# Kernel optimization log

Hardware: AMD Instinct MI355X
Metric: run time of the kernel (lower is better)

Reference implementation:

```python
import jax, jax.numpy as jnp
import numpy as np

N, D, K = 32768, 256, 8192
SQRT3 = 3.0 ** 0.5


def setup_inputs() -> dict:
    key = jax.random.key(0)
    k1, k2 = jax.random.split(key)
    x = jax.random.normal(k1, (N, D), dtype=jnp.float32)
    # torch .uniform_(-sqrt(3), sqrt(3)) on an [D, K] table
    embeddings = jax.random.uniform(k2, (D, K), dtype=jnp.float32,
                                    minval=-SQRT3, maxval=SQRT3)
    return {"x": x, "embeddings": embeddings}


def reference(x, embeddings):
    # x: [N, D] (forward flattens from dim 1; 2D input is identity)
    # embeddings: [D, K]
    # squared L2 distances: ||y||^2 - 2 y.E + ||e||^2  -> [N, K]
    dist = (jnp.sum(x * x, axis=1, keepdims=True)
            - 2.0 * (x @ embeddings)
            + jnp.sum(embeddings * embeddings, axis=0, keepdims=True))
    idx = jnp.argmin(dist, axis=1)  # [N]
    # one_hot(idx) @ E^T == gather of columns of E (same math, no dense one-hot)
    quantized = jnp.take(embeddings, idx, axis=1).T  # [N, D]
    return quantized.reshape(x.shape)
```

## Files before the change

### kernel.cpp

```cpp
#include <hip/hip_runtime.h>
#include <math.h>
#include <float.h>

#define N_ROWS 32768
#define D_DIM  256
#define K_DIM  8192

#define EPS1 0.40f
#define EPS2 0.02f
#define T2CAP 4096
#define T3CAP 512
#define NSPLIT3 16

typedef _Float16 f16;
typedef _Float16 f16x8 __attribute__((ext_vector_type(8)));
typedef float f32x4 __attribute__((ext_vector_type(4)));

#define KSPLIT 8
#define COLS_PER_SPLIT (K_DIM / KSPLIT)
#define CHUNK_COLS 32
#define NCHUNK (COLS_PER_SPLIT / CHUNK_COLS)

__global__ void convx_kernel(const float* __restrict__ X, f16* __restrict__ X16) {
    const size_t i = ((size_t)blockIdx.x * 256 + threadIdx.x) * 8;
    float4 a = *reinterpret_cast<const float4*>(X + i);
    float4 b = *reinterpret_cast<const float4*>(X + i + 4);
    f16x8 o;
    o[0]=(f16)a.x; o[1]=(f16)a.y; o[2]=(f16)a.z; o[3]=(f16)a.w;
    o[4]=(f16)b.x; o[5]=(f16)b.y; o[6]=(f16)b.z; o[7]=(f16)b.w;
    *reinterpret_cast<f16x8*>(X16 + i) = o;
}

__global__ void packe_kernel(const float* __restrict__ E, f16* __restrict__ Epack) {
    const int gid = blockIdx.x * 256 + threadIdx.x;
    const int l    = gid & 63;
    const int t    = (gid >> 6) & 7;
    const int tile = gid >> 9;
    const int k  = 16 * tile + (l & 15);
    const int d0 = 32 * t + (l >> 4) * 8;
    f16x8 o;
#pragma unroll
    for (int j = 0; j < 8; ++j) o[j] = (f16)E[(size_t)(d0 + j) * K_DIM + k];
    *reinterpret_cast<f16x8*>(Epack + (size_t)gid * 8) = o;
}

__global__ void nhen_kernel(const float* __restrict__ E, float* __restrict__ nhen) {
    const int k = blockIdx.x * 256 + threadIdx.x;
    float s = 0.0f;
#pragma unroll 8
    for (int d = 0; d < D_DIM; ++d) {
        float v = E[(size_t)d * K_DIM + k];
        s = fmaf(v, v, s);
    }
    nhen[k] = -0.5f * s;
}

__global__ void transpose_kernel(const float* __restrict__ E, float* __restrict__ ET) {
    __shared__ float t[64][65];
    const int bk = blockIdx.x & (K_DIM / 64 - 1);
    const int bd = blockIdx.x >> 7;
    const int c  = threadIdx.x & 63;
    const int r0 = (threadIdx.x >> 6) * 16;
    const int d0 = bd * 64, k0 = bk * 64;
#pragma unroll
    for (int i = 0; i < 16; ++i)
        t[r0 + i][c] = E[(size_t)(d0 + r0 + i) * K_DIM + k0 + c];
    __syncthreads();
#pragma unroll
    for (int i = 0; i < 16; ++i)
        ET[(size_t)(k0 + r0 + i) * D_DIM + d0 + c] = t[c][r0 + i];
}

__launch_bounds__(256, 2)
__global__ void pass1_kernel(const f16* __restrict__ X16,
                             const f16* __restrict__ Epack,
                             const float* __restrict__ nhen,
                             float* __restrict__ p_best,
                             float* __restrict__ p_sec,
                             int*   __restrict__ p_idx) {
    __shared__ f16 B_lds[2][8192];

    const int tid = threadIdx.x;
    const int wv = tid >> 6;
    const int lane = tid & 63;
    const int l15 = lane & 15;
    const int l4  = lane >> 4;
    const int rg = blockIdx.x >> 3;
    const int ks = blockIdx.x & 7;
    const int rowW = rg * 256 + wv * 64;
    const int colBase = ks * COLS_PER_SPLIT;

    f16x8 A[4][8];
#pragma unroll
    for (int rt = 0; rt < 4; ++rt)
#pragma unroll
        for (int t = 0; t < 8; ++t)
            A[rt][t] = *reinterpret_cast<const f16x8*>(
                X16 + (size_t)(rowW + 16*rt + l15) * D_DIM + 32*t + l4*8);

    float best[16], sec[16];
    int bbase[16];
#pragma unroll
    for (int s = 0; s < 16; ++s) { best[s] = -INFINITY; sec[s] = -INFINITY; bbase[s] = 0; }

    const float4* src = reinterpret_cast<const float4*>(
        Epack + (size_t)colBase * 256);

    float4 sreg[4];
#pragma unroll
    for (int q = 0; q < 4; ++q) sreg[q] = src[q*256 + tid];
    {
        float4* bw = reinterpret_cast<float4*>(&B_lds[0][0]);
#pragma unroll
        for (int q = 0; q < 4; ++q) bw[q*256 + tid] = sreg[q];
    }

    for (int ci = 0; ci < NCHUNK; ++ci) {
        __syncthreads();
        if (ci + 1 < NCHUNK) {
#pragma unroll
            for (int q = 0; q < 4; ++q)
                sreg[q] = src[(size_t)(ci+1)*1024 + q*256 + tid];
        }
        const f16* bufc = &B_lds[ci & 1][0];
        const int c0 = colBase + ci * CHUNK_COLS;

#pragma unroll
        for (int ct = 0; ct < 2; ++ct) {
            const float nh = nhen[c0 + 16*ct + l15];
            const f32x4 nh4 = {nh, nh, nh, nh};
            f32x4 acc[4];
            {
                f16x8 B = *reinterpret_cast<const f16x8*>(bufc + (ct*8)*512 + lane*8);
#pragma unroll
                for (int rt = 0; rt < 4; ++rt)
                    acc[rt] = __builtin_amdgcn_mfma_f32_16x16x32_f16(A[rt][0], B, nh4, 0, 0, 0);
            }
#pragma unroll
            for (int t = 1; t < 8; ++t) {
                f16x8 B = *reinterpret_cast<const f16x8*>(bufc + (ct*8 + t)*512 + lane*8);
#pragma unroll
                for (int rt = 0; rt < 4; ++rt)
                    acc[rt] = __builtin_amdgcn_mfma_f32_16x16x32_f16(A[rt][t], B, acc[rt], 0, 0, 0);
            }
#pragma unroll
            for (int rt = 0; rt < 4; ++rt) {
#pragma unroll
                for (int r = 0; r < 4; ++r) {
                    const float v = acc[rt][r];
                    const int sl = rt*4 + r;
                    sec[sl] = __builtin_amdgcn_fmed3f(v, best[sl], sec[sl]);
                    const bool gt = v > best[sl];
                    best[sl] = gt ? v : best[sl];
                    bbase[sl] = gt ? (c0 + 16*ct) : bbase[sl];
                }
            }
        }

        if (ci + 1 < NCHUNK) {
            float4* bw = reinterpret_cast<float4*>(&B_lds[(ci+1) & 1][0]);
#pragma unroll
            for (int q = 0; q < 4; ++q) bw[q*256 + tid] = sreg[q];
        }
    }

#pragma unroll
    for (int s = 0; s < 16; ++s) {
        float b = best[s], sc = sec[s];
        int k = bbase[s] + l15;
#pragma unroll
        for (int off = 8; off >= 1; off >>= 1) {
            float ob = __shfl_xor(b, off, 16);
            float os = __shfl_xor(sc, off, 16);
            int   ok = __shfl_xor(k, off, 16);
            float sm = fmaxf(fmaxf(sc, os), fminf(b, ob));
            bool take = (ob > b) || (ob == b && ok < k);
            b = take ? ob : b;
            k = take ? ok : k;
            sc = sm;
        }
        if (l15 == 0) {
            const int row = rowW + 16*(s >> 2) + 4*l4 + (s & 3);
            p_best[ks * N_ROWS + row] = b;
            p_sec [ks * N_ROWS + row] = sc;
            p_idx [ks * N_ROWS + row] = k;
        }
    }
}

__global__ void zero_counts_kernel(int* count, int* count3) { *count = 0; *count3 = 0; }

__global__ void merge_kernel(const float* __restrict__ p_best,
                             const float* __restrict__ p_sec,
                             const int*   __restrict__ p_idx,
                             int* __restrict__ idxf,
                             int* __restrict__ list, int* __restrict__ count) {
    const int n = blockIdx.x * 256 + threadIdx.x;
    float b = p_best[n], sc = p_sec[n];
    int k = p_idx[n];
#pragma unroll
    for (int s = 1; s < KSPLIT; ++s) {
        float ob = p_best[s * N_ROWS + n];
        float os = p_sec [s * N_ROWS + n];
        int   ok = p_idx [s * N_ROWS + n];
        float sm = fmaxf(fmaxf(sc, os), fminf(b, ob));
        bool take = ob > b;
        b = take ? ob : b; k = take ? ok : k; sc = sm;
    }
    idxf[n] = k;
    if (2.0f * (b - sc) < EPS1) {
        int pos = atomicAdd(count, 1);
        if (pos < T2CAP) list[pos] = n;
    }
}

__launch_bounds__(256, 2)
__global__ void tier2_kernel(const float* __restrict__ X,
                             const float* __restrict__ E,
                             const float* __restrict__ nhen,
                             const int* __restrict__ list,
                             const int* __restrict__ count,
                             float* __restrict__ t2b, float* __restrict__ t2s,
                             int* __restrict__ t2i) {
    const int g  = blockIdx.x >> 4;
    const int sp = blockIdx.x & 15;
    const int cnt = min(*count, T2CAP);
    if (g * 64 >= cnt) return;

    __shared__ float xT[D_DIM][64];
    __shared__ float es[64][64];
    const int tid = threadIdx.x;
    const int tx = tid & 15, ty = tid >> 4;

    {
        const int r = tid >> 2;
        const int slot = min(g * 64 + r, cnt - 1);
        const int row = list[slot];
        const int d0 = (tid & 3) * 64;
        const float* xp = X + (size_t)row * D_DIM + d0;
#pragma unroll
        for (int i = 0; i < 64; i += 4) {
            float4 v = *reinterpret_cast<const float4*>(xp + i);
            xT[d0+i+0][r] = v.x; xT[d0+i+1][r] = v.y;
            xT[d0+i+2][r] = v.z; xT[d0+i+3][r] = v.w;
        }
    }

    float best[4], sec[4]; int bidx[4];
#pragma unroll
    for (int i = 0; i < 4; ++i) { best[i] = -INFINITY; sec[i] = -INFINITY; bidx[i] = 0; }

    const int colBase = sp * 512;
    for (int kc = 0; kc < 512; kc += 64) {
        float acc[4][4];
#pragma unroll
        for (int i = 0; i < 4; ++i)
#pragma unroll
            for (int j = 0; j < 4; ++j) acc[i][j] = 0.0f;

        for (int dc = 0; dc < D_DIM; dc += 64) {
            __syncthreads();
#pragma unroll
            for (int dd = 0; dd < 64; dd += 16) {
                int d = dd + (tid >> 4);
                float4 v = *reinterpret_cast<const float4*>(
                    &E[(size_t)(dc + d) * K_DIM + colBase + kc + (tid & 15) * 4]);
                *reinterpret_cast<float4*>(&es[d][(tid & 15) * 4]) = v;
            }
            __syncthreads();
#pragma unroll 8
            for (int d = 0; d < 64; ++d) {
                float4 xv = *reinterpret_cast<const float4*>(&xT[dc + d][ty * 4]);
                float4 ev = *reinterpret_cast<const float4*>(&es[d][tx * 4]);
                float xr[4] = {xv.x, xv.y, xv.z, xv.w};
                float ec[4] = {ev.x, ev.y, ev.z, ev.w};
#pragma unroll
                for (int i = 0; i < 4; ++i)
#pragma unroll
                    for (int j = 0; j < 4; ++j)
                        acc[i][j] = fmaf(xr[i], ec[j], acc[i][j]);
            }
        }
        float4 nhv = *reinterpret_cast<const float4*>(&nhen[colBase + kc + tx * 4]);
        float nh[4] = {nhv.x, nhv.y, nhv.z, nhv.w};
#pragma unroll
        for (int j = 0; j < 4; ++j) {
            const int k = colBase + kc + tx * 4 + j;
#pragma unroll
            for (int i = 0; i < 4; ++i) {
                float u = nh[j] + acc[i][j];
                bool gt = u > best[i];
                sec[i]  = fmaxf(sec[i], fminf(u, best[i]));
                best[i] = gt ? u : best[i];
                bidx[i] = gt ? k : bidx[i];
            }
        }
    }

#pragma unroll
    for (int off = 8; off >= 1; off >>= 1) {
#pragma unroll
        for (int i = 0; i < 4; ++i) {
            float ob = __shfl_xor(best[i], off, 16);
            float os = __shfl_xor(sec[i], off, 16);
            int   ok = __shfl_xor(bidx[i], off, 16);
            float sm = fmaxf(fmaxf(sec[i], os), fminf(best[i], ob));
            bool take = (ob > best[i]) || (ob == best[i] && ok < bidx[i]);
            best[i] = take ? ob : best[i];
            bidx[i] = take ? ok : bidx[i];
            sec[i] = sm;
        }
    }
    if (tx == 0) {
#pragma unroll
        for (int i = 0; i < 4; ++i) {
            const int slot = g * 64 + ty * 4 + i;
            if (slot < cnt) {
                t2b[sp * T2CAP + slot] = best[i];
                t2s[sp * T2CAP + slot] = sec[i];
                t2i[sp * T2CAP + slot] = bidx[i];
            }
        }
    }
}

__global__ void merge2_kernel(const float* __restrict__ t2b,
                              const float* __restrict__ t2s,
                              const int*   __restrict__ t2i,
                              const int* __restrict__ list,
                              const int* __restrict__ count,
                              int* __restrict__ idxf,
                              int* __restrict__ list3, int* __restrict__ count3) {
    const int slot = blockIdx.x * 256 + threadIdx.x;
    const int cnt = min(*count, T2CAP);
    if (slot >= cnt) return;
    float b = t2b[slot], sc = t2s[slot];
    int k = t2i[slot];
#pragma unroll
    for (int sp = 1; sp < 16; ++sp) {
        float ob = t2b[sp * T2CAP + slot];
        float os = t2s[sp * T2CAP + slot];
        int   ok = t2i[sp * T2CAP + slot];
        float sm = fmaxf(fmaxf(sc, os), fminf(b, ob));
        bool take = ob > b;
        b = take ? ob : b; k = take ? ok : k; sc = sm;
    }
    const int n = list[slot];
    idxf[n] = k;
    if (2.0f * (b - sc) < EPS2) {
        int pos = atomicAdd(count3, 1);
        if (pos < T3CAP) list3[pos] = n;
    }
}

__launch_bounds__(256)
__global__ void tier3_kernel(const float* __restrict__ X,
                             const float* __restrict__ E,
                             const int* __restrict__ list3,
                             const int* __restrict__ count3,
                             double* __restrict__ t3b, int* __restrict__ t3i) {
    const int slot = blockIdx.x >> 4;
    const int sp   = blockIdx.x & 15;
    const int cnt = min(*count3, T3CAP);
    if (slot >= cnt) return;
    const int n = list3[slot];

    __shared__ float xs[D_DIM];
    const int tid = threadIdx.x;
    xs[tid] = X[(size_t)n * D_DIM + tid];
    __syncthreads();

    const int colBase = sp * 512;
    double best = DBL_MAX;
    int bi = 0x7fffffff;
#pragma unroll
    for (int kk = 0; kk < 512; kk += 256) {
        const int k = colBase + kk + tid;
        double s0 = 0.0, s1 = 0.0, s2 = 0.0, s3 = 0.0;
#pragma unroll 4
        for (int d = 0; d < D_DIM; d += 4) {
            double f0 = (double)xs[d+0] - (double)E[(size_t)(d+0) * K_DIM + k];
            double f1 = (double)xs[d+1] - (double)E[(size_t)(d+1) * K_DIM + k];
            double f2 = (double)xs[d+2] - (double)E[(size_t)(d+2) * K_DIM + k];
            double f3 = (double)xs[d+3] - (double)E[(size_t)(d+3) * K_DIM + k];
            s0 = fma(f0, f0, s0); s1 = fma(f1, f1, s1);
            s2 = fma(f2, f2, s2); s3 = fma(f3, f3, s3);
        }
        double s = (s0 + s1) + (s2 + s3);
        if (s < best) { best = s; bi = k; }
    }

    __shared__ double bv[256];
    __shared__ int bix[256];
    bv[tid] = best; bix[tid] = bi;
    __syncthreads();
    if (tid == 0) {
        double b = bv[0]; int ix = bix[0];
        for (int t = 1; t < 256; ++t)
            if (bv[t] < b || (bv[t] == b && bix[t] < ix)) { b = bv[t]; ix = bix[t]; }
        t3b[sp * T3CAP + slot] = b;
        t3i[sp * T3CAP + slot] = ix;
    }
}

__global__ void merge3_kernel(const double* __restrict__ t3b,
                              const int* __restrict__ t3i,
                              const int* __restrict__ list3,
                              const int* __restrict__ count3,
                              int* __restrict__ idxf) {
    const int slot = blockIdx.x * 256 + threadIdx.x;
    const int cnt = min(*count3, T3CAP);
    if (slot >= cnt) return;
    double b = t3b[slot];
    int k = t3i[slot];
#pragma unroll
    for (int sp = 1; sp < NSPLIT3; ++sp) {
        double ob = t3b[sp * T3CAP + slot];
        int   ok = t3i[sp * T3CAP + slot];
        if (ob < b || (ob == b && ok < k)) { b = ob; k = ok; }
    }
    idxf[list3[slot]] = k;
}

__global__ void gather2_kernel(const float* __restrict__ ET,
                               const int* __restrict__ idx,
                               float* __restrict__ out) {
    const int n  = blockIdx.x * 4 + (threadIdx.x >> 6);
    const int d4 = (threadIdx.x & 63) * 4;
    const int k  = idx[n];
    *reinterpret_cast<float4*>(&out[(size_t)n * D_DIM + d4]) =
        *reinterpret_cast<const float4*>(&ET[(size_t)k * D_DIM + d4]);
}

__global__ void gather_kernel(const float* __restrict__ E,
                              const int* __restrict__ idx,
                              float* __restrict__ out) {
    const int n = blockIdx.x;
    const int d = threadIdx.x;
    const int k = idx[n];
    out[(size_t)n * D_DIM + d] = E[(size_t)d * K_DIM + k];
}

__global__ void fb_enorm_kernel(const float* __restrict__ E, float* __restrict__ enorm) {
    int k = blockIdx.x * 256 + threadIdx.x;
    float s = 0.0f;
#pragma unroll 8
    for (int d = 0; d < D_DIM; ++d) { float v = E[(size_t)d * K_DIM + k]; s = fmaf(v, v, s); }
    enorm[k] = s;
}

__launch_bounds__(256, 2)
__global__ void fb_dist_kernel(const float* __restrict__ X, const float* __restrict__ E,
                               const float* __restrict__ enorm,
                               int* __restrict__ idx_out, float* __restrict__ gap_out) {
    __shared__ float xT[D_DIM][64];
    __shared__ float es[64][64];
    const int tid = threadIdx.x;
    const int tx = tid & 15, ty = tid >> 4;
    const int rowBase = blockIdx.x * 64;
    {
        const int r = tid >> 2;
        const int d0 = (tid & 3) * 64;
        const float* xp = X + (size_t)(rowBase + r) * D_DIM + d0;
#pragma unroll
        for (int i = 0; i < 64; i += 4) {
            float4 v = *reinterpret_cast<const float4*>(xp + i);
            xT[d0+i+0][r]=v.x; xT[d0+i+1][r]=v.y; xT[d0+i+2][r]=v.z; xT[d0+i+3][r]=v.w;
        }
    }
    float bestVal[4], secVal[4]; int bestIdx[4];
#pragma unroll
    for (int i = 0; i < 4; ++i) { bestVal[i]=INFINITY; secVal[i]=INFINITY; bestIdx[i]=0; }
    for (int kc = 0; kc < K_DIM; kc += 64) {
        float acc[4][4];
#pragma unroll
        for (int i=0;i<4;++i)
#pragma unroll
            for (int j=0;j<4;++j) acc[i][j]=0.f;
        for (int dc = 0; dc < D_DIM; dc += 64) {
            __syncthreads();
#pragma unroll
            for (int dd = 0; dd < 64; dd += 16) {
                int d = dd + (tid >> 4);
                float4 v = *reinterpret_cast<const float4*>(
                    &E[(size_t)(dc+d)*K_DIM + kc + (tid&15)*4]);
                *reinterpret_cast<float4*>(&es[d][(tid&15)*4]) = v;
            }
            __syncthreads();
#pragma unroll 8
            for (int d = 0; d < 64; ++d) {
                float4 xv = *reinterpret_cast<const float4*>(&xT[dc+d][ty*4]);
                float4 ev = *reinterpret_cast<const float4*>(&es[d][tx*4]);
                float xr[4]={xv.x,xv.y,xv.z,xv.w}, ec[4]={ev.x,ev.y,ev.z,ev.w};
#pragma unroll
                for (int i=0;i<4;++i)
#pragma unroll
                    for (int j=0;j<4;++j) acc[i][j]=fmaf(xr[i],ec[j],acc[i][j]);
            }
        }
        float4 env = *reinterpret_cast<const float4*>(&enorm[kc + tx*4]);
        float en[4]={env.x,env.y,env.z,env.w};
#pragma unroll
        for (int j=0;j<4;++j) {
            int k = kc + tx*4 + j;
#pragma unroll
            for (int i=0;i<4;++i) {
                float s = fmaf(-2.0f, acc[i][j], en[j]);
                if (s < bestVal[i]) { secVal[i]=bestVal[i]; bestVal[i]=s; bestIdx[i]=k; }
                else if (s < secVal[i]) secVal[i]=s;
            }
        }
    }
#pragma unroll
    for (int off=8; off>=1; off>>=1) {
#pragma unroll
        for (int i=0;i<4;++i) {
            float oB=__shfl_xor(bestVal[i],off,16);
            int oI=__shfl_xor(bestIdx[i],off,16);
            float oS=__shfl_xor(secVal[i],off,16);
            float ms=fminf(fminf(secVal[i],oS),fmaxf(bestVal[i],oB));
            if (oB<bestVal[i] || (oB==bestVal[i] && oI<bestIdx[i])) { bestVal[i]=oB; bestIdx[i]=oI; }
            secVal[i]=ms;
        }
    }
    if (tx==0) {
#pragma unroll
        for (int i=0;i<4;++i) {
            idx_out[rowBase + ty*4 + i] = bestIdx[i];
            gap_out[rowBase + ty*4 + i] = secVal[i]-bestVal[i];
        }
    }
}

__launch_bounds__(256)
__global__ void fb_refine_kernel(const float* __restrict__ X, const float* __restrict__ E,
                                 const float* __restrict__ gap, int* __restrict__ idx) {
    const int n = blockIdx.x;
    if (gap[n] >= 0.0625f) return;
    __shared__ float xs[D_DIM];
    const int tid = threadIdx.x;
    xs[tid] = X[(size_t)n * D_DIM + tid];
    __syncthreads();
    double best = DBL_MAX; int bi = 0x7fffffff;
    for (int k = tid; k < K_DIM; k += 256) {
        double s0=0,s1=0,s2=0,s3=0;
#pragma unroll 4
        for (int d = 0; d < D_DIM; d += 4) {
            double f0=(double)xs[d+0]-(double)E[(size_t)(d+0)*K_DIM+k];
            double f1=(double)xs[d+1]-(double)E[(size_t)(d+1)*K_DIM+k];
            double f2=(double)xs[d+2]-(double)E[(size_t)(d+2)*K_DIM+k];
            double f3=(double)xs[d+3]-(double)E[(size_t)(d+3)*K_DIM+k];
            s0=fma(f0,f0,s0); s1=fma(f1,f1,s1); s2=fma(f2,f2,s2); s3=fma(f3,f3,s3);
        }
        double s=(s0+s1)+(s2+s3);
        if (s<best){best=s;bi=k;}
    }
    __shared__ double bv[256]; __shared__ int bix[256];
    bv[tid]=best; bix[tid]=bi;
    __syncthreads();
    if (tid==0) {
        double b=bv[0]; int ix=bix[0];
        for (int t=1;t<256;++t)
            if (bv[t]<b || (bv[t]==b && bix[t]<ix)) { b=bv[t]; ix=bix[t]; }
        idx[n]=ix;
    }
}

extern "C" void kernel_launch(void* const* d_in, const int* in_sizes, int n_in,
                              void* d_out, int out_size, void* d_ws, size_t ws_size,
                              hipStream_t stream) {
    const float* X = (const float*)d_in[0];
    const float* E = (const float*)d_in[1];
    float* out = (float*)d_out;
    char* ws = (char*)d_ws;

    const size_t o_nhen  = 0;
    const size_t o_pb    = 32768;
    const size_t o_ps    = o_pb  + (size_t)KSPLIT * N_ROWS * 4;
    const size_t o_pi    = o_ps  + (size_t)KSPLIT * N_ROWS * 4;
    const size_t o_idx   = o_pi  + (size_t)KSPLIT * N_ROWS * 4;
    const size_t o_list  = o_idx + (size_t)N_ROWS * 4;
    const size_t o_count = o_list + (size_t)T2CAP * 4;
    const size_t o_t2b   = o_count + 256;
    const size_t o_t2s   = o_t2b + (size_t)16 * T2CAP * 4;
    const size_t o_t2i   = o_t2s + (size_t)16 * T2CAP * 4;
    const size_t o_list3 = o_t2i + (size_t)16 * T2CAP * 4;
    const size_t o_t3b   = o_list3 + (size_t)T3CAP * 4;
    const size_t o_t3i   = o_t3b + (size_t)NSPLIT3 * T3CAP * 8;
    const size_t o_x16   = o_t3i + (size_t)NSPLIT3 * T3CAP * 4;
    const size_t o_epack = o_x16 + (size_t)N_ROWS * D_DIM * 2;
    const size_t NEED_BASE = o_epack + (size_t)D_DIM * K_DIM * 2;
    const size_t o_et    = NEED_BASE;
    const size_t NEED_FULL = o_et + (size_t)D_DIM * K_DIM * 4;

    if (ws_size >= NEED_BASE) {
        float*  nhen  = (float*) (ws + o_nhen);
        float*  p_b   = (float*) (ws + o_pb);
        float*  p_s   = (float*) (ws + o_ps);
        int*    p_i   = (int*)   (ws + o_pi);
        int*    idxf  = (int*)   (ws + o_idx);
        int*    list  = (int*)   (ws + o_list);
        int*    count = (int*)   (ws + o_count);
        int*    count3= (int*)   (ws + o_count + 4);
        float*  t2b   = (float*) (ws + o_t2b);
        float*  t2s   = (float*) (ws + o_t2s);
        int*    t2i   = (int*)   (ws + o_t2i);
        int*    list3 = (int*)   (ws + o_list3);
        double* t3b   = (double*)(ws + o_t3b);
        int*    t3i   = (int*)   (ws + o_t3i);
        f16*    X16   = (f16*)   (ws + o_x16);
        f16*    Epack = (f16*)   (ws + o_epack);
        float*  ET    = (float*) (ws + o_et);
        const bool haveET = ws_size >= NEED_FULL;

        convx_kernel<<<(N_ROWS * D_DIM / 8) / 256, 256, 0, stream>>>(X, X16);
        packe_kernel<<<(K_DIM / 16) * 8 * 64 / 256, 256, 0, stream>>>(E, Epack);
        nhen_kernel<<<K_DIM / 256, 256, 0, stream>>>(E, nhen);
        if (haveET)
            transpose_kernel<<<(K_DIM / 64) * (D_DIM / 64), 256, 0, stream>>>(E, ET);
        zero_counts_kernel<<<1, 1, 0, stream>>>(count, count3);
        pass1_kernel<<<(N_ROWS / 256) * KSPLIT, 256, 0, stream>>>(
            X16, Epack, nhen, p_b, p_s, p_i);
        merge_kernel<<<N_ROWS / 256, 256, 0, stream>>>(
            p_b, p_s, p_i, idxf, list, count);
        tier2_kernel<<<(T2CAP / 64) * 16, 256, 0, stream>>>(
            X, E, nhen, list, count, t2b, t2s, t2i);
        merge2_kernel<<<T2CAP / 256, 256, 0, stream>>>(
            t2b, t2s, t2i, list, count, idxf, list3, count3);
        tier3_kernel<<<T3CAP * NSPLIT3, 256, 0, stream>>>(
            X, E, list3, count3, t3b, t3i);
        merge3_kernel<<<T3CAP / 256, 256, 0, stream>>>(
            t3b, t3i, list3, count3, idxf);
        if (haveET)
            gather2_kernel<<<N_ROWS / 4, 256, 0, stream>>>(ET, idxf, out);
        else
            gather_kernel<<<N_ROWS, 256, 0, stream>>>(E, idxf, out);
    } else {
        float* enorm = (float*)ws;
        int*   idx   = (int*)(ws + 32768);
        float* gap   = (float*)(ws + 32768 + (size_t)N_ROWS * 4);
        fb_enorm_kernel<<<K_DIM / 256, 256, 0, stream>>>(E, enorm);
        fb_dist_kernel<<<N_ROWS / 64, 256, 0, stream>>>(X, E, enorm, idx, gap);
        fb_refine_kernel<<<N_ROWS, 256, 0, stream>>>(X, E, gap, idx);
        gather_kernel<<<N_ROWS, 256, 0, stream>>>(E, idx, out);
    }
}
```

Measured before the change: 365.3 us.

## Stage codebook chunks with direct global-to-LDS loads and wider chunks

Replaces the register-staged double buffer in pass1 with `global_load_lds` copies that write the packed codebook straight into shared memory. The chunk width doubles from 32 to 64 columns, so there are half as many barrier-separated iterations and each iteration does twice the MFMA work. This frees the staging registers and removes the separate LDS store phase. In exchange, LDS per block doubles to 64KB, and correctness now depends on the barrier waiting for the asynchronous LDS writes to finish.

```diff
diff --git a/kernel.cpp b/kernel.cpp
--- a/kernel.cpp
+++ b/kernel.cpp
@@ -18,8 +18,16 @@
 
 #define KSPLIT 8
 #define COLS_PER_SPLIT (K_DIM / KSPLIT)
-#define CHUNK_COLS 32
+#define CHUNK_COLS 64
 #define NCHUNK (COLS_PER_SPLIT / CHUNK_COLS)
+#define CHUNK_BYTES (CHUNK_COLS * D_DIM * 2)
+
+typedef unsigned int u32;
+typedef const u32 __attribute__((address_space(1)))* gas1_u32;
+typedef u32 __attribute__((address_space(3)))* las3_u32;
+__device__ __forceinline__ void gload_lds16(const void* g, void* l) {
+    __builtin_amdgcn_global_load_lds((gas1_u32)g, (las3_u32)l, 16, 0, 0);
+}
 
 __global__ void convx_kernel(const float* __restrict__ X, f16* __restrict__ X16) {
     const size_t i = ((size_t)blockIdx.x * 256 + threadIdx.x) * 8;
@@ -78,7 +86,7 @@
                              float* __restrict__ p_best,
                              float* __restrict__ p_sec,
                              int*   __restrict__ p_idx) {
-    __shared__ f16 B_lds[2][8192];
+    __shared__ f16 B_lds[2][CHUNK_BYTES / 2];
 
     const int tid = threadIdx.x;
     const int wv = tid >> 6;
@@ -103,30 +111,29 @@
 #pragma unroll
     for (int s = 0; s < 16; ++s) { best[s] = -INFINITY; sec[s] = -INFINITY; bbase[s] = 0; }
 
-    const float4* src = reinterpret_cast<const float4*>(
-        Epack + (size_t)colBase * 256);
-
-    float4 sreg[4];
-#pragma unroll
-    for (int q = 0; q < 4; ++q) sreg[q] = src[q*256 + tid];
-    {
-        float4* bw = reinterpret_cast<float4*>(&B_lds[0][0]);
-#pragma unroll
-        for (int q = 0; q < 4; ++q) bw[q*256 + tid] = sreg[q];
-    }
+    const char* splitSrc = (const char*)Epack + (size_t)colBase * 512;
+
+    auto STAGE = [&](int b, int ci) {
+        const char* csrc = splitSrc + (size_t)ci * CHUNK_BYTES;
+        char* cdst = (char*)&B_lds[b][0];
+#pragma unroll
+        for (int c = 0; c < 8; ++c) {
+            const int seg = wv * 8 + c;
+            gload_lds16(csrc + seg * 1024 + (lane << 4), cdst + seg * 1024);
+        }
+    };
+
+    STAGE(0, 0);
 
     for (int ci = 0; ci < NCHUNK; ++ci) {
         __syncthreads();
-        if (ci + 1 < NCHUNK) {
-#pragma unroll
-            for (int q = 0; q < 4; ++q)
-                sreg[q] = src[(size_t)(ci+1)*1024 + q*256 + tid];
-        }
+        if (ci + 1 < NCHUNK) STAGE((ci + 1) & 1, ci + 1);
+
         const f16* bufc = &B_lds[ci & 1][0];
         const int c0 = colBase + ci * CHUNK_COLS;
 
 #pragma unroll
-        for (int ct = 0; ct < 2; ++ct) {
+        for (int ct = 0; ct < 4; ++ct) {
             const float nh = nhen[c0 + 16*ct + l15];
             const f32x4 nh4 = {nh, nh, nh, nh};
             f32x4 acc[4];
@@ -155,12 +162,6 @@
                     bbase[sl] = gt ? (c0 + 16*ct) : bbase[sl];
                 }
             }
-        }
-
-        if (ci + 1 < NCHUNK) {
-            float4* bw = reinterpret_cast<float4*>(&B_lds[(ci+1) & 1][0]);
-#pragma unroll
-            for (int q = 0; q < 4; ++q) bw[q*256 + tid] = sreg[q];
         }
     }
 
```

Measured after the change: 370.2 us. About the same (+1.3%).
